# Performance work log

Measured on AMD Instinct MI355X. Metric: run time of the kernel, lower is better.

## Reference

```python
import jax, jax.numpy as jnp
import numpy as np

B, T, D, S, H, OUT, V = 8, 1024, 128, 8, 4, 32000, 128000
Dh = D // H


def setup_inputs() -> dict:
    key = jax.random.key(0)
    ks = jax.random.split(key, 16)
    n = jax.random.normal
    p = {}
    p["x"] = jax.random.randint(ks[0], (B, T), 0, V)
    p["emb"] = n(ks[1], (V, D), dtype=jnp.float32) * 0.02          # embedding table
    p["init_states"] = n(ks[2], (1, S, D), dtype=jnp.float32)      # learned initial states
    p["Wz"] = n(ks[3], (D, 2 * D)) * 0.05; p["bz"] = jnp.zeros((D,))
    p["Wr"] = n(ks[4], (D, 2 * D)) * 0.05; p["br"] = jnp.zeros((D,))
    p["Wh"] = n(ks[5], (D, 2 * D)) * 0.05; p["bh"] = jnp.zeros((D,))
    p["Wq"] = n(ks[6], (D, D)) * 0.05; p["bq"] = jnp.zeros((D,))
    p["Wk"] = n(ks[7], (D, D)) * 0.05; p["bk"] = jnp.zeros((D,))
    p["Wv"] = n(ks[8], (D, D)) * 0.05; p["bv"] = jnp.zeros((D,))
    p["Wo"] = n(ks[9], (D, D)) * 0.05; p["bo"] = jnp.zeros((D,))
    p["Wc"] = n(ks[10], (D, 2 * D)) * 0.05; p["bc"] = jnp.zeros((D,))
    p["Wout"] = n(ks[11], (OUT, S * D)) * 0.02; p["bout"] = jnp.zeros((OUT,))
    return p


def reference(x, emb, init_states, Wz, bz, Wr, br, Wh, bh, Wq, bq, Wk, bk, Wv, bv, Wo, bo, Wc, bc, Wout, bout):
    xe = emb[x]  # [B,T,D] token embeddings
    scale = 1.0 / jnp.sqrt(jnp.asarray(Dh, xe.dtype))

    def mha(s):  # multi-head self-attention across the S state tokens; s: [B,S,D]
        q = (s @ Wq.T + bq).reshape(B, S, H, Dh)
        k = (s @ Wk.T + bk).reshape(B, S, H, Dh)
        v = (s @ Wv.T + bv).reshape(B, S, H, Dh)
        att = jax.nn.softmax(jnp.einsum('bqhd,bkhd->bhqk', q, k) * scale, axis=-1)
        o = jnp.einsum('bhqk,bkhd->bqhd', att, v).reshape(B, S, D)
        return o @ Wo.T + bo

    def step(states, xt):  # states: [B,S,D], xt: [B,D]
        inp = jnp.broadcast_to(xt[:, None, :], (B, S, D))  # input_t.repeat(1, num_states, 1)
        comb = jnp.concatenate([states, inp], axis=-1)
        z = jax.nn.sigmoid(comb @ Wz.T + bz)                # update gate
        r = jax.nn.sigmoid(comb @ Wr.T + br)                # reset gate
        cand = jnp.tanh(jnp.concatenate([r * states, inp], axis=-1) @ Wh.T + bh)
        new = (1.0 - z) * states + z * cand                 # GRU-style state update
        attn = mha(new)                                     # inter-state communication
        g = jax.nn.sigmoid(jnp.concatenate([new, attn], axis=-1) @ Wc.T + bc)
        new = g * new + (1.0 - g) * attn                    # gated communication blend
        return new, None

    states0 = jnp.broadcast_to(init_states, (B, S, D))
    states, _ = jax.lax.scan(step, states0, jnp.swapaxes(xe, 0, 1))  # scan over T
    return states.reshape(B, S * D) @ Wout.T + bout  # [B, OUT]
```

## Files before the change

kernel.cpp:

```cpp
#include <hip/hip_runtime.h>
#include <math.h>

#define NB 8
#define NT 1024
#define ND 128
#define NS 8
#define NH 4
#define NOUT 32000

typedef _Float16 f16x8 __attribute__((ext_vector_type(8)));
typedef float f32x4 __attribute__((ext_vector_type(4)));

__device__ __forceinline__ float sigm(float x) { return 1.0f / (1.0f + __expf(-x)); }
__device__ __forceinline__ float ftanh(float x) {
    float ax = fabsf(x);
    float e = __expf(-2.0f * ax);
    float t = (1.0f - e) / (1.0f + e);
    return copysignf(t, x);
}
__device__ __forceinline__ float dot4(float4 a, float4 b) {
    return a.x * b.x + a.y * b.y + a.z * b.z + a.w * b.w;
}

#define QPADD(v, ctrl)                                                             \
    (v) += __int_as_float(__builtin_amdgcn_update_dpp(                             \
        0, __float_as_int(v), (ctrl), 0xF, 0xF, true))

#define BAR()                                              \
    {                                                      \
        asm volatile("s_waitcnt lgkmcnt(0)" ::: "memory"); \
        __builtin_amdgcn_s_barrier();                      \
        asm volatile("" ::: "memory");                     \
    }

__global__ __launch_bounds__(128) void k_wow(
    const float* __restrict__ Wo, const float* __restrict__ Wv,
    const float* __restrict__ bv, float* __restrict__ Wow, float* __restrict__ bvo) {
    int j = blockIdx.x;
    int k = threadIdx.x;
    __shared__ float woj[ND];
    woj[k] = Wo[j * ND + k];
    __syncthreads();
    float acc = 0.f;
#pragma unroll 8
    for (int d = 0; d < ND; ++d) acc += woj[d] * Wv[d * ND + k];
    Wow[j * ND + k] = acc;
    if (k == 0) {
        float s = 0.f;
        for (int d = 0; d < ND; ++d) s += bv[d] * woj[d];
        bvo[j] = s;
    }
}

__global__ __launch_bounds__(256) void k_pack(
    const float* __restrict__ Wz, const float* __restrict__ Wr, const float* __restrict__ Wh,
    const float* __restrict__ Wq, const float* __restrict__ Wk, const float* __restrict__ Wow,
    const float* __restrict__ Wc, _Float16* __restrict__ wpack) {
    int linear = blockIdx.x * 256 + threadIdx.x;
    int m = linear >> 12;
    int rem = linear & 4095;
    int f = rem >> 9;
    int t = rem & 511;
    int kt = f >> 1, pl = f & 1;
    int w = t >> 6, lane = t & 63;
    int col = 16 * w + (lane & 15);
    int kk = kt * 32 + 8 * (lane >> 4);
    const float* src;
    int stride, koff = 0;
    switch (m) {
        case 0: src = Wz; stride = 256; break;
        case 1: src = Wr; stride = 256; break;
        case 2: src = Wh; stride = 256; break;
        case 3: src = Wq; stride = 128; break;
        case 4: src = Wk; stride = 128; break;
        case 5: src = Wow; stride = 128; break;
        case 6: src = Wc; stride = 256; break;
        default: src = Wc; stride = 256; koff = 128; break;
    }
    const float* p = src + (size_t)col * stride + koff + kk;
    f16x8 out;
#pragma unroll
    for (int i = 0; i < 8; ++i) {
        float v = p[i];
        _Float16 h = (_Float16)v;
        out[i] = pl ? (_Float16)((v - (float)h) * 2048.0f) : h;
    }
    *(f16x8*)(wpack + (size_t)linear * 8) = out;
}

__global__ __launch_bounds__(128) void k_embed_xproj(
    const int* __restrict__ x, const float* __restrict__ emb,
    const float* __restrict__ Wz, const float* __restrict__ bz,
    const float* __restrict__ Wr, const float* __restrict__ br,
    const float* __restrict__ Wh, const float* __restrict__ bh,
    float* __restrict__ xproj) {
    int bt = blockIdx.x;
    int j = threadIdx.x;
    __shared__ float xe[ND];
    long tok = (long)x[bt];
    xe[j] = emb[tok * ND + j];
    __syncthreads();
    const float4* xe4 = (const float4*)xe;
    const float4* wz = (const float4*)(Wz + j * 2 * ND + ND);
    const float4* wr = (const float4*)(Wr + j * 2 * ND + ND);
    const float4* wh = (const float4*)(Wh + j * 2 * ND + ND);
    float az = bz[j], ar = br[j], ah = bh[j];
#pragma unroll 8
    for (int k = 0; k < ND / 4; ++k) {
        float4 xv = xe4[k];
        az += dot4(wz[k], xv);
        ar += dot4(wr[k], xv);
        ah += dot4(wh[k], xv);
    }
    float* o = xproj + (long)bt * 3 * ND;
    o[j] = az;
    o[ND + j] = ar;
    o[2 * ND + j] = ah;
}

__global__ __launch_bounds__(512, 2) void k_scan(
    const float* __restrict__ xproj, const float* __restrict__ init_states,
    const _Float16* __restrict__ wpack, const float* __restrict__ bvo,
    const float* __restrict__ bq, const float* __restrict__ bk,
    const float* __restrict__ bo, const float* __restrict__ bc,
    float* __restrict__ stout) {
    const int b = blockIdx.x, tid = threadIdx.x;
    const int lane = tid & 63, w = tid >> 6;
    const int lrow = lane & 15, lkb = lane >> 4;
    const int c = 16 * w + lrow;
    const bool vrow = (lkb < 2);

    __shared__ float qf[NS][132], kf[NS][132];
    __shared__ float vofT[ND][8];
    __shared__ float pf[8][NS][NS];
    __shared__ _Float16 hp[8][8 * 128];
    __shared__ f16x8 wzh[2048], wrh[2048], whh[2048], wqh[2048];

#define LOADW(BH, BL, m)                                                          \
    {                                                                             \
        const f16x8* base_ = (const f16x8*)wpack + ((m) << 12);                   \
        _Pragma("unroll") for (int kt_ = 0; kt_ < 4; ++kt_) {                     \
            BH[kt_] = base_[((kt_ * 2 + 0) << 9) + tid];                          \
            BL[kt_] = base_[((kt_ * 2 + 1) << 9) + tid];                          \
        }                                                                         \
    }

#define LDA(ph, pl_)                                                              \
    {                                                                             \
        _Pragma("unroll") for (int kt_ = 0; kt_ < 4; ++kt_) {                     \
            int off_ = ((lrow & 7) * 256 + kt_ * 64 + lkb * 16) ^ ((lrow & 7) << 4); \
            ah[kt_] = *(const f16x8*)((const char*)(ph) + off_);                  \
            al[kt_] = *(const f16x8*)((const char*)(pl_) + off_);                 \
        }                                                                         \
    }

#define MM(res, BH, BL, init0)                                                    \
    {                                                                             \
        f32x4 xh_ = {(init0), (init0), (init0), (init0)};                         \
        f32x4 xl_ = {0.f, 0.f, 0.f, 0.f};                                         \
        _Pragma("unroll") for (int kt_ = 0; kt_ < 4; ++kt_) {                     \
            xh_ = __builtin_amdgcn_mfma_f32_16x16x32_f16(ah[kt_], BH[kt_], xh_, 0, 0, 0); \
            xl_ = __builtin_amdgcn_mfma_f32_16x16x32_f16(al[kt_], BH[kt_], xl_, 0, 0, 0); \
            xl_ = __builtin_amdgcn_mfma_f32_16x16x32_f16(ah[kt_], BL[kt_], xl_, 0, 0, 0); \
        }                                                                         \
        _Pragma("unroll") for (int i_ = 0; i_ < 4; ++i_)                          \
            res[i_] = xh_[i_] + xl_[i_] * 4.8828125e-4f;                          \
    }

#define MM_HL(res, WH, m, init0)                                                  \
    {                                                                             \
        const f16x8* base_ = (const f16x8*)wpack + ((m) << 12);                   \
        f32x4 xh_ = {(init0), (init0), (init0), (init0)};                         \
        f32x4 xl_ = {0.f, 0.f, 0.f, 0.f};                                         \
        _Pragma("unroll") for (int kt_ = 0; kt_ < 4; ++kt_) {                     \
            f16x8 bh_ = WH[(kt_ << 9) + tid];                                     \
            f16x8 bl_ = base_[((kt_ * 2 + 1) << 9) + tid];                        \
            xh_ = __builtin_amdgcn_mfma_f32_16x16x32_f16(ah[kt_], bh_, xh_, 0, 0, 0); \
            xl_ = __builtin_amdgcn_mfma_f32_16x16x32_f16(al[kt_], bh_, xl_, 0, 0, 0); \
            xl_ = __builtin_amdgcn_mfma_f32_16x16x32_f16(ah[kt_], bl_, xl_, 0, 0, 0); \
        }                                                                         \
        _Pragma("unroll") for (int i_ = 0; i_ < 4; ++i_)                          \
            res[i_] = xh_[i_] + xl_[i_] * 4.8828125e-4f;                          \
    }

#define WRHL(pih, pil, row_, col_, val_)                                          \
    {                                                                             \
        float v_ = (val_);                                                        \
        _Float16 h_ = (_Float16)v_;                                               \
        _Float16 l_ = (_Float16)((v_ - (float)h_) * 2048.0f);                     \
        int off_ = ((row_)*256 + (col_)*2) ^ (((row_)&7) << 4);                   \
        *(_Float16*)((char*)hp[pih] + off_) = h_;                                 \
        *(_Float16*)((char*)hp[pil] + off_) = l_;                                 \
    }

    {
        const f16x8* wp8 = (const f16x8*)wpack;
        for (int i = tid; i < 2048; i += 512) {
            int kt = i >> 9, tt = i & 511;
            wzh[i] = wp8[(0 << 12) + ((kt * 2 + 0) << 9) + tt];
            wrh[i] = wp8[(1 << 12) + ((kt * 2 + 0) << 9) + tt];
            whh[i] = wp8[(2 << 12) + ((kt * 2 + 0) << 9) + tt];
            wqh[i] = wp8[(3 << 12) + ((kt * 2 + 0) << 9) + tt];
        }
    }

    float stv[4];
#pragma unroll
    for (int i = 0; i < 4; ++i) {
        int r = 4 * lkb + i;
        float v = init_states[(r & 7) * ND + c];
        stv[i] = v;
        if (vrow) WRHL(0, 1, r, c, v);
    }

    f16x8 Bkh[4], Bkl[4];
    LOADW(Bkh, Bkl, 4);
    f16x8 Sh[4], Sl[4];
    LOADW(Sh, Sl, 5);

    const float bqv = bq[c], bkv = bk[c], bvoc = bvo[c], bov = bo[c], bcv = bc[c];
    const float scale = 0.17677669529663687f;

    f16x8 ah[4], al[4];
    float zv[4], nwv[4];
    f32x4 ach, acl;

    const float* xpb = xproj + ((size_t)b * NT) * 3 * ND;
    float xz = xpb[c], xr = xpb[ND + c], xh = xpb[2 * ND + c];

    BAR();

    for (int t = 0; t < NT; ++t) {
        LDA(hp[0], hp[1]);
        float zp[4], rp[4];
        MM_HL(zp, wzh, 0, xz);
        MM_HL(rp, wrh, 1, xr);
#pragma unroll
        for (int i = 0; i < 4; ++i) zv[i] = sigm(zp[i]);
        if (vrow) {
#pragma unroll
            for (int i = 0; i < 4; ++i) {
                float rs_ = sigm(rp[i]) * stv[i];
                WRHL(2, 3, 4 * lkb + i, c, rs_);
            }
        }
        BAR();
        LDA(hp[2], hp[3]);
        float hpre[4];
        MM_HL(hpre, whh, 2, xh);
#pragma unroll
        for (int i = 0; i < 4; ++i) {
            float cand = ftanh(hpre[i]);
            float nv = (1.0f - zv[i]) * stv[i] + zv[i] * cand;
            nwv[i] = nv;
        }
        if (vrow) {
#pragma unroll
            for (int i = 0; i < 4; ++i) WRHL(4, 5, 4 * lkb + i, c, nwv[i]);
        }
        BAR();
        LDA(hp[4], hp[5]);
        {
            float qp[4];
            MM_HL(qp, wqh, 3, bqv);
            if (vrow) {
#pragma unroll
                for (int i = 0; i < 4; ++i) qf[4 * lkb + i][c] = qp[i];
            }
            float kp[4];
            MM(kp, Bkh, Bkl, bkv);
            if (vrow) {
#pragma unroll
                for (int i = 0; i < 4; ++i) kf[4 * lkb + i][c] = kp[i];
            }
            float vp[4];
            MM(vp, Sh, Sl, bvoc);
            LOADW(Sh, Sl, 6);
            if (vrow) {
                float4 vv;
                vv.x = vp[0]; vv.y = vp[1]; vv.z = vp[2]; vv.w = vp[3];
                *(float4*)&vofT[c][4 * lkb] = vv;
            }
        }
        BAR();
        {
            int hh = w >> 1;
            int sq = lane >> 3, skv = lane & 7;
            float s_ = 0.f;
#pragma unroll
            for (int j = 0; j < 8; ++j) {
                float4 qv = *(const float4*)&qf[sq][32 * hh + 4 * j];
                float4 kv4 = *(const float4*)&kf[skv][32 * hh + 4 * j];
                s_ += dot4(qv, kv4);
            }
            s_ *= scale;
            float e_ = __expf(s_);
            float sm = e_;
            QPADD(sm, 0xB1);
            QPADD(sm, 0x4E);
            sm += __shfl_xor(sm, 4);
            pf[w][sq][skv] = e_ / sm;
        }
        ach = (f32x4){bcv, bcv, bcv, bcv};
        acl = (f32x4){0.f, 0.f, 0.f, 0.f};
#pragma unroll
        for (int kt_ = 0; kt_ < 4; ++kt_) {
            ach = __builtin_amdgcn_mfma_f32_16x16x32_f16(ah[kt_], Sh[kt_], ach, 0, 0, 0);
            acl = __builtin_amdgcn_mfma_f32_16x16x32_f16(al[kt_], Sh[kt_], acl, 0, 0, 0);
            acl = __builtin_amdgcn_mfma_f32_16x16x32_f16(ah[kt_], Sl[kt_], acl, 0, 0, 0);
        }
        LOADW(Sh, Sl, 7);
        if (vrow) {
            float4 voa = *(const float4*)&vofT[c][0];
            float4 vob = *(const float4*)&vofT[c][4];
#pragma unroll
            for (int i = 0; i < 4; ++i) {
                int r = 4 * lkb + i, pq = r & 7;
                float4 pa = *(const float4*)&pf[w][pq][0];
                float4 pb = *(const float4*)&pf[w][pq][4];
                float acc = bov + dot4(pa, voa) + dot4(pb, vob);
                WRHL(6, 7, r, c, acc);
            }
        }
        BAR();
        LDA(hp[6], hp[7]);
#pragma unroll
        for (int kt_ = 0; kt_ < 4; ++kt_) {
            ach = __builtin_amdgcn_mfma_f32_16x16x32_f16(ah[kt_], Sh[kt_], ach, 0, 0, 0);
            acl = __builtin_amdgcn_mfma_f32_16x16x32_f16(al[kt_], Sh[kt_], acl, 0, 0, 0);
            acl = __builtin_amdgcn_mfma_f32_16x16x32_f16(ah[kt_], Sl[kt_], acl, 0, 0, 0);
        }
        LOADW(Sh, Sl, 5);
        if (vrow) {
#pragma unroll
            for (int i = 0; i < 4; ++i) {
                int r = 4 * lkb + i;
                int off_ = (r * 256 + c * 2) ^ ((r & 7) << 4);
                float hi = (float)*(_Float16*)((char*)hp[6] + off_);
                float lo = (float)*(_Float16*)((char*)hp[7] + off_);
                float atv = hi + lo * 4.8828125e-4f;
                float g = sigm(ach[i] + acl[i] * 4.8828125e-4f);
                float sv = g * nwv[i] + (1.0f - g) * atv;
                stv[i] = sv;
                WRHL(0, 1, r, c, sv);
            }
        }
        {
            int tn = (t + 1 < NT) ? t + 1 : t;
            const float* xpn = xproj + ((size_t)(b * NT + tn)) * 3 * ND;
            xz = xpn[c];
            xr = xpn[ND + c];
            xh = xpn[2 * ND + c];
        }
        BAR();
    }
    if (vrow) {
#pragma unroll
        for (int i = 0; i < 4; ++i) {
            int r = 4 * lkb + i;
            stout[(size_t)b * NS * ND + r * ND + c] = stv[i];
        }
    }
#undef LOADW
#undef LDA
#undef MM
#undef MM_HL
#undef WRHL
}

__global__ __launch_bounds__(512) void k_out(
    const float* __restrict__ stflat, const float* __restrict__ Wout,
    const float* __restrict__ bout, float* __restrict__ out) {
    __shared__ float stl[NB][NS * ND];
    int tid = threadIdx.x;
    for (int idx = tid; idx < NB * NS * ND; idx += 512)
        stl[idx >> 10][idx & 1023] = stflat[idx];
    __syncthreads();
    int wave = tid >> 6, lane = tid & 63;
    int o = blockIdx.x * 8 + wave;
    float acc[NB];
#pragma unroll
    for (int b = 0; b < NB; ++b) acc[b] = 0.0f;
    const float4* wrow = (const float4*)(Wout + (size_t)o * (NS * ND));
#pragma unroll
    for (int i = 0; i < 4; ++i) {
        float4 wv = wrow[i * 64 + lane];
        int kb = (i * 64 + lane) * 4;
#pragma unroll
        for (int b = 0; b < NB; ++b) {
            float4 sv = *(const float4*)&stl[b][kb];
            acc[b] += dot4(wv, sv);
        }
    }
#pragma unroll
    for (int off = 32; off; off >>= 1) {
#pragma unroll
        for (int b = 0; b < NB; ++b) acc[b] += __shfl_down(acc[b], off);
    }
    if (lane == 0) {
        float bb = bout[o];
#pragma unroll
        for (int b = 0; b < NB; ++b) out[(size_t)b * NOUT + o] = acc[b] + bb;
    }
}

extern "C" void kernel_launch(void* const* d_in, const int* in_sizes, int n_in,
                              void* d_out, int out_size, void* d_ws, size_t ws_size,
                              hipStream_t stream) {
    const int* x = (const int*)d_in[0];
    const float* emb = (const float*)d_in[1];
    const float* init_states = (const float*)d_in[2];
    const float* Wz = (const float*)d_in[3];
    const float* bz = (const float*)d_in[4];
    const float* Wr = (const float*)d_in[5];
    const float* br = (const float*)d_in[6];
    const float* Wh = (const float*)d_in[7];
    const float* bh = (const float*)d_in[8];
    const float* Wq = (const float*)d_in[9];
    const float* bq = (const float*)d_in[10];
    const float* Wk = (const float*)d_in[11];
    const float* bk = (const float*)d_in[12];
    const float* Wv = (const float*)d_in[13];
    const float* bv = (const float*)d_in[14];
    const float* Wo = (const float*)d_in[15];
    const float* bo = (const float*)d_in[16];
    const float* Wc = (const float*)d_in[17];
    const float* bc = (const float*)d_in[18];
    const float* Wout = (const float*)d_in[19];
    const float* bout = (const float*)d_in[20];
    float* out = (float*)d_out;

    float* xproj = (float*)d_ws;
    float* stflat = xproj + (size_t)NB * NT * 3 * ND;
    _Float16* wpack = (_Float16*)(stflat + NB * NS * ND);
    float* Wow = (float*)(wpack + (size_t)8 * 4096 * 8);
    float* bvo = Wow + ND * ND;

    k_wow<<<ND, ND, 0, stream>>>(Wo, Wv, bv, Wow, bvo);
    k_pack<<<128, 256, 0, stream>>>(Wz, Wr, Wh, Wq, Wk, Wow, Wc, wpack);
    k_embed_xproj<<<NB * NT, 128, 0, stream>>>(x, emb, Wz, bz, Wr, br, Wh, bh, xproj);
    k_scan<<<NB, 512, 0, stream>>>(xproj, init_states, wpack, bvo, bq, bk, bo, bc, stflat);
    k_out<<<NOUT / 8, 512, 0, stream>>>(stflat, Wout, bout, out);
}
```

Measured before the change: 6.546 ms.

## Fold attention output projection into gate weights to drop a scan barrier

Precomputes Wc2·Wo·Wv (Wcw) and a folded bias so the gate's attention contribution is a per-step V-side projection combined with the softmax probabilities, instead of materialising the attention output and running a second MFMA pass over it. This removes one block-wide barrier, one LDS round-trip and one weight-chunk matmul per time step in the serial scan. In exchange each step runs an extra 128x128 projection on the state, keeps another weight set resident in registers (more register pressure), and adds a small setup kernel.

```diff
diff --git a/kernel.cpp b/kernel.cpp
--- a/kernel.cpp
+++ b/kernel.cpp
@@ -52,10 +52,31 @@
     }
 }
 
+__global__ __launch_bounds__(128) void k_wcw(
+    const float* __restrict__ Wc, const float* __restrict__ Wow,
+    const float* __restrict__ bvo, const float* __restrict__ bo,
+    float* __restrict__ Wcw, float* __restrict__ bcb) {
+    int j = blockIdx.x;
+    int k = threadIdx.x;
+    __shared__ float wc2[ND];
+    wc2[k] = Wc[j * 2 * ND + ND + k];
+    __syncthreads();
+    float acc = 0.f;
+#pragma unroll 8
+    for (int d = 0; d < ND; ++d) acc += wc2[d] * Wow[d * ND + k];
+    Wcw[j * ND + k] = acc;
+    if (k == 0) {
+        float s = 0.f;
+        for (int d = 0; d < ND; ++d) s += (bvo[d] + bo[d]) * wc2[d];
+        bcb[j] = s;
+    }
+}
+
 __global__ __launch_bounds__(256) void k_pack(
     const float* __restrict__ Wz, const float* __restrict__ Wr, const float* __restrict__ Wh,
     const float* __restrict__ Wq, const float* __restrict__ Wk, const float* __restrict__ Wow,
-    const float* __restrict__ Wc, _Float16* __restrict__ wpack) {
+    const float* __restrict__ Wcw, const float* __restrict__ Wc,
+    _Float16* __restrict__ wpack) {
     int linear = blockIdx.x * 256 + threadIdx.x;
     int m = linear >> 12;
     int rem = linear & 4095;
@@ -75,7 +96,7 @@
         case 4: src = Wk; stride = 128; break;
         case 5: src = Wow; stride = 128; break;
         case 6: src = Wc; stride = 256; break;
-        default: src = Wc; stride = 256; koff = 128; break;
+        default: src = Wcw; stride = 128; break;
     }
     const float* p = src + (size_t)col * stride + koff + kk;
     f16x8 out;
@@ -121,6 +142,7 @@
 __global__ __launch_bounds__(512, 2) void k_scan(
     const float* __restrict__ xproj, const float* __restrict__ init_states,
     const _Float16* __restrict__ wpack, const float* __restrict__ bvo,
+    const float* __restrict__ bcb,
     const float* __restrict__ bq, const float* __restrict__ bk,
     const float* __restrict__ bo, const float* __restrict__ bc,
     float* __restrict__ stout) {
@@ -131,9 +153,9 @@
     const bool vrow = (lkb < 2);
 
     __shared__ float qf[NS][132], kf[NS][132];
-    __shared__ float vofT[ND][8];
+    __shared__ float vofT[ND][8], vcT[ND][8];
     __shared__ float pf[8][NS][NS];
-    __shared__ _Float16 hp[8][8 * 128];
+    __shared__ _Float16 hp[6][8 * 128];
     __shared__ f16x8 wzh[2048], wrh[2048], whh[2048], wqh[2048];
 
 #define LOADW(BH, BL, m)                                                          \
@@ -215,10 +237,12 @@
 
     f16x8 Bkh[4], Bkl[4];
     LOADW(Bkh, Bkl, 4);
-    f16x8 Sh[4], Sl[4];
-    LOADW(Sh, Sl, 5);
-
-    const float bqv = bq[c], bkv = bk[c], bvoc = bvo[c], bov = bo[c], bcv = bc[c];
+    f16x8 S0h[4], S0l[4], S1h[4], S1l[4];
+    LOADW(S0h, S0l, 5);
+    LOADW(S1h, S1l, 7);
+
+    const float bqv = bq[c], bkv = bk[c], bvoc = bvo[c], bov = bo[c];
+    const float bcv = bc[c], bcbc = bcb[c];
     const float scale = 0.17677669529663687f;
 
     f16x8 ah[4], al[4];
@@ -274,12 +298,20 @@
                 for (int i = 0; i < 4; ++i) kf[4 * lkb + i][c] = kp[i];
             }
             float vp[4];
-            MM(vp, Sh, Sl, bvoc);
-            LOADW(Sh, Sl, 6);
+            MM(vp, S0h, S0l, bvoc);
+            LOADW(S0h, S0l, 6);
             if (vrow) {
                 float4 vv;
                 vv.x = vp[0]; vv.y = vp[1]; vv.z = vp[2]; vv.w = vp[3];
                 *(float4*)&vofT[c][4 * lkb] = vv;
+            }
+            float vcp[4];
+            MM(vcp, S1h, S1l, 0.0f);
+            LOADW(S1h, S1l, 7);
+            if (vrow) {
+                float4 vv;
+                vv.x = vcp[0]; vv.y = vcp[1]; vv.z = vcp[2]; vv.w = vcp[3];
+                *(float4*)&vcT[c][4 * lkb] = vv;
             }
         }
         BAR();
@@ -305,42 +337,25 @@
         acl = (f32x4){0.f, 0.f, 0.f, 0.f};
 #pragma unroll
         for (int kt_ = 0; kt_ < 4; ++kt_) {
-            ach = __builtin_amdgcn_mfma_f32_16x16x32_f16(ah[kt_], Sh[kt_], ach, 0, 0, 0);
-            acl = __builtin_amdgcn_mfma_f32_16x16x32_f16(al[kt_], Sh[kt_], acl, 0, 0, 0);
-            acl = __builtin_amdgcn_mfma_f32_16x16x32_f16(ah[kt_], Sl[kt_], acl, 0, 0, 0);
-        }
-        LOADW(Sh, Sl, 7);
+            ach = __builtin_amdgcn_mfma_f32_16x16x32_f16(ah[kt_], S0h[kt_], ach, 0, 0, 0);
+            acl = __builtin_amdgcn_mfma_f32_16x16x32_f16(al[kt_], S0h[kt_], acl, 0, 0, 0);
+            acl = __builtin_amdgcn_mfma_f32_16x16x32_f16(ah[kt_], S0l[kt_], acl, 0, 0, 0);
+        }
+        LOADW(S0h, S0l, 5);
         if (vrow) {
             float4 voa = *(const float4*)&vofT[c][0];
             float4 vob = *(const float4*)&vofT[c][4];
+            float4 vca = *(const float4*)&vcT[c][0];
+            float4 vcb = *(const float4*)&vcT[c][4];
 #pragma unroll
             for (int i = 0; i < 4; ++i) {
                 int r = 4 * lkb + i, pq = r & 7;
                 float4 pa = *(const float4*)&pf[w][pq][0];
                 float4 pb = *(const float4*)&pf[w][pq][4];
-                float acc = bov + dot4(pa, voa) + dot4(pb, vob);
-                WRHL(6, 7, r, c, acc);
-            }
-        }
-        BAR();
-        LDA(hp[6], hp[7]);
-#pragma unroll
-        for (int kt_ = 0; kt_ < 4; ++kt_) {
-            ach = __builtin_amdgcn_mfma_f32_16x16x32_f16(ah[kt_], Sh[kt_], ach, 0, 0, 0);
-            acl = __builtin_amdgcn_mfma_f32_16x16x32_f16(al[kt_], Sh[kt_], acl, 0, 0, 0);
-            acl = __builtin_amdgcn_mfma_f32_16x16x32_f16(ah[kt_], Sl[kt_], acl, 0, 0, 0);
-        }
-        LOADW(Sh, Sl, 5);
-        if (vrow) {
-#pragma unroll
-            for (int i = 0; i < 4; ++i) {
-                int r = 4 * lkb + i;
-                int off_ = (r * 256 + c * 2) ^ ((r & 7) << 4);
-                float hi = (float)*(_Float16*)((char*)hp[6] + off_);
-                float lo = (float)*(_Float16*)((char*)hp[7] + off_);
-                float atv = hi + lo * 4.8828125e-4f;
-                float g = sigm(ach[i] + acl[i] * 4.8828125e-4f);
-                float sv = g * nwv[i] + (1.0f - g) * atv;
+                float at_ = bov + dot4(pa, voa) + dot4(pb, vob);
+                float cv_ = dot4(pa, vca) + dot4(pb, vcb);
+                float g_ = sigm(ach[i] + acl[i] * 4.8828125e-4f + bcbc + cv_);
+                float sv = g_ * nwv[i] + (1.0f - g_) * at_;
                 stv[i] = sv;
                 WRHL(0, 1, r, c, sv);
             }
@@ -435,10 +450,14 @@
     _Float16* wpack = (_Float16*)(stflat + NB * NS * ND);
     float* Wow = (float*)(wpack + (size_t)8 * 4096 * 8);
     float* bvo = Wow + ND * ND;
+    float* Wcw = bvo + ND;
+    float* bcb = Wcw + ND * ND;
 
     k_wow<<<ND, ND, 0, stream>>>(Wo, Wv, bv, Wow, bvo);
-    k_pack<<<128, 256, 0, stream>>>(Wz, Wr, Wh, Wq, Wk, Wow, Wc, wpack);
+    k_wcw<<<ND, ND, 0, stream>>>(Wc, Wow, bvo, bo, Wcw, bcb);
+    k_pack<<<128, 256, 0, stream>>>(Wz, Wr, Wh, Wq, Wk, Wow, Wcw, Wc, wpack);
     k_embed_xproj<<<NB * NT, 128, 0, stream>>>(x, emb, Wz, bz, Wr, br, Wh, bh, xproj);
-    k_scan<<<NB, 512, 0, stream>>>(xproj, init_states, wpack, bvo, bq, bk, bo, bc, stflat);
+    k_scan<<<NB, 512, 0, stream>>>(xproj, init_states, wpack, bvo, bcb, bq, bk, bo, bc,
+                                   stflat);
     k_out<<<NOUT / 8, 512, 0, stream>>>(stflat, Wout, bout, out);
 }
```

New measurement: 8.627 ms. 1.32x slower.
